# Performance work log

Measured on AMD Instinct MI355X. Metric: run time of the kernel, lower is better.

Reference implementation:

```python
import jax, jax.numpy as jnp
import numpy as np

NH, DK, DV, CHUNK = 4, 256, 256, 32
HID = 1024
FLOOR = 0.05
EPS = 1e-5


def _l2norm(x):
    return x * jax.lax.rsqrt(jnp.sum(x * x, -1, keepdims=True) + 1e-6)


def _causal_dw_conv(x, w):
    # x: (B,L,D), w: (D,K) depthwise causal FIR conv
    K = w.shape[-1]
    y = jax.lax.conv_general_dilated(
        jnp.swapaxes(x, 1, 2), w[:, None, :], (1,), [(K - 1, 0)],
        dimension_numbers=('NCH', 'OIH', 'NCH'), feature_group_count=w.shape[0])
    return jnp.swapaxes(y, 1, 2)


def _fir(x, w):
    # x: (B,L,H,D), w: (H,D,K)
    B, L, H, D = x.shape
    return _causal_dw_conv(x.reshape(B, L, H * D), w.reshape(H * D, -1)).reshape(B, L, H, D)


def _stats(x):
    mean = jnp.mean(x, -1, keepdims=True)
    var = jnp.var(x, -1, keepdims=True)
    am = jnp.mean(jnp.abs(x), -1, keepdims=True)
    l2 = jnp.linalg.norm(x, axis=-1, keepdims=True)
    return jnp.concatenate([mean, var, am, l2], -1)


def _delta_rule(q, k, v, beta, c=CHUNK):
    # q,k: (b,h,L,dk), v: (b,h,L,dv), beta: (b,h,L); L % c == 0
    b, h, L, dk = q.shape
    dv = v.shape[-1]
    q = _l2norm(q)
    k = _l2norm(k)
    v = v * beta[..., None]
    kb = k * beta[..., None]
    n = L // c
    rs = lambda t: t.reshape(b, h, n, c, -1)
    q, k, v, kb = rs(q), rs(k), rs(v), rs(kb)
    strict_low = jnp.tril(jnp.ones((c, c), bool), -1)
    attn = -(kb @ jnp.swapaxes(k, -1, -2)) * strict_low
    col = jnp.arange(c)
    def row_body(i, a):
        upd = jnp.einsum('...k,...kj->...j', a[..., i, :], a)
        return a.at[..., i, :].add(jnp.where(col < i, upd, 0.0))
    attn_inv = jax.lax.fori_loop(1, c, row_body, attn) + jnp.eye(c, dtype=attn.dtype)
    u = attn_inv @ v    # (b,h,n,c,dv)
    w = attn_inv @ kb   # (b,h,n,c,dk)
    incl_low = jnp.tril(jnp.ones((c, c), bool))
    def step(S, xs):
        q_i, k_i, u_i, w_i = xs
        attn_loc = jnp.einsum('bhid,bhjd->bhij', q_i, k_i) * incl_low
        u_i = u_i - w_i @ S
        o_i = q_i @ S + attn_loc @ u_i
        return S + jnp.swapaxes(k_i, -1, -2) @ u_i, o_i
    mv = lambda t: jnp.moveaxis(t, 2, 0)
    S0 = jnp.zeros((b, h, dk, dv), q.dtype)
    S, o = jax.lax.scan(step, S0, (mv(q), mv(k), mv(u), mv(w)))
    return jnp.moveaxis(o, 0, 2).reshape(b, h, L, dv), S


def setup_inputs() -> dict:
    key = jax.random.key(0)
    ks = jax.random.split(key, 16)
    B, L = 2, 4096
    s = 0.02
    hs = jax.random.normal(ks[0], (B, L, HID), jnp.float32)
    Wq = jax.random.normal(ks[1], (HID, NH * DK)) * s
    Wk = jax.random.normal(ks[2], (HID, NH * DK)) * s
    Wv = jax.random.normal(ks[3], (HID, NH * DV)) * s
    Wb = jax.random.normal(ks[4], (HID, NH)) * s
    conv_q_w = jax.random.normal(ks[5], (NH * DK, 4)) * 0.1
    conv_k_w = jax.random.normal(ks[6], (NH * DK, 4)) * 0.1
    conv_v_w = jax.random.normal(ks[7], (NH * DV, 4)) * 0.1
    fir_short_w = jnp.zeros((NH, DV, 5)).at[..., -1].set(1.0) + jax.random.normal(ks[8], (NH, DV, 5)) * 0.02
    fir_long_w = jnp.zeros((NH, DV, 64)).at[..., -1].set(1.0) + jax.random.normal(ks[9], (NH, DV, 64)) * 0.02
    gin, hg = HID + 16, HID * 2 // 2
    mlp_w1 = jax.random.normal(ks[10], (gin, hg)) * s
    mlp_b1 = jnp.zeros((hg,), jnp.float32)
    mlp_w2 = jax.random.normal(ks[11], (hg, 4)) * s
    mlp_b2 = jnp.array([-0.5, -0.5, 0.5, 1.5], jnp.float32)
    log_temp = jnp.zeros((NH, 1), jnp.float32)
    o_norm_w = jnp.ones((DV,), jnp.float32)
    Wo = jax.random.normal(ks[12], (NH * DV, HID)) * s
    return dict(hidden_states=hs, Wq=Wq, Wk=Wk, Wv=Wv, Wb=Wb, conv_q_w=conv_q_w,
                conv_k_w=conv_k_w, conv_v_w=conv_v_w, fir_short_w=fir_short_w,
                fir_long_w=fir_long_w, mlp_w1=mlp_w1, mlp_b1=mlp_b1, mlp_w2=mlp_w2,
                mlp_b2=mlp_b2, log_temp=log_temp, o_norm_w=o_norm_w, Wo=Wo)


def reference(hidden_states, Wq, Wk, Wv, Wb, conv_q_w, conv_k_w, conv_v_w,
              fir_short_w, fir_long_w, mlp_w1, mlp_b1, mlp_w2, mlp_b2,
              log_temp, o_norm_w, Wo):
    B, L, _ = hidden_states.shape
    # projections + causal short conv (silu) as in ShortConvolution
    q = jax.nn.silu(_causal_dw_conv(hidden_states @ Wq, conv_q_w)).reshape(B, L, NH, DK)
    k = jax.nn.silu(_causal_dw_conv(hidden_states @ Wk, conv_k_w)).reshape(B, L, NH, DK)
    v_direct = jax.nn.silu(_causal_dw_conv(hidden_states @ Wv, conv_v_w)).reshape(B, L, NH, DV)
    beta = jax.nn.sigmoid(hidden_states @ Wb)  # (B,L,NH)
    bhld = lambda t: jnp.transpose(t, (0, 2, 1, 3))
    delta_bh, _ = _delta_rule(bhld(q), bhld(k), bhld(v_direct), jnp.transpose(beta, (0, 2, 1)))
    delta_out = jnp.transpose(delta_bh, (0, 2, 1, 3))  # (B,L,NH,DV)
    local_short = _fir(v_direct, fir_short_w)
    local_long = _fir(v_direct, fir_long_w)
    stats_vec = jnp.concatenate([_stats(local_short), _stats(local_long),
                                 _stats(delta_out), _stats(v_direct)], -1)  # (B,L,NH,16)
    hs_exp = jnp.broadcast_to(hidden_states[:, :, None, :], (B, L, NH, HID))
    gate_in = jnp.concatenate([hs_exp, stats_vec], -1)
    h1 = jax.nn.gelu(gate_in @ mlp_w1 + mlp_b1, approximate=False)
    logits = h1 @ mlp_w2 + mlp_b2  # (B,L,NH,4)
    probs = jax.nn.softmax(logits / jnp.exp(log_temp), -1)
    probs = FLOOR + (1.0 - 4.0 * FLOOR) * probs  # min-floor fusion weights
    o = (probs[..., 0:1] * local_short + probs[..., 1:2] * local_long
         + probs[..., 2:3] * delta_out + probs[..., 3:4] * v_direct)
    o = o * jax.lax.rsqrt(jnp.mean(o * o, -1, keepdims=True) + EPS) * o_norm_w  # RMSNorm per head
    return o.reshape(B, L, NH * DV) @ Wo
```

## Files before the change

### kernel.cpp

```cpp
#include <hip/hip_runtime.h>
#include <hip/hip_bf16.h>

#define NTOK 8192
#define HID 1024
#define NH 4
#define DK 256
#define DV 256
#define SEQ 4096
#define NCHUNK 128

#define BM 128
#define BN 128
#define BKK 16
__global__ __launch_bounds__(256) void gemm_f32(const float* __restrict__ A,
    const float* __restrict__ B, float* __restrict__ C, int M, int N, int K) {
  __shared__ __align__(16) float As[BKK][BM + 4];
  __shared__ __align__(16) float Bs[BKK][BN + 4];
  int tid = threadIdx.x;
  int bm = blockIdx.y * BM, bn = blockIdx.x * BN;
  int tx = tid & 15, ty = tid >> 4;
  float acc[8][8];
  #pragma unroll
  for (int i = 0; i < 8; ++i)
    #pragma unroll
    for (int j = 0; j < 8; ++j) acc[i][j] = 0.f;
  for (int k0 = 0; k0 < K; k0 += BKK) {
    #pragma unroll
    for (int jj = 0; jj < 2; ++jj) {
      int v = tid + (jj << 8);
      int row = v >> 2, kk = (v & 3) << 2;
      float4 a = *(const float4*)&A[(size_t)(bm + row) * K + k0 + kk];
      As[kk + 0][row] = a.x; As[kk + 1][row] = a.y;
      As[kk + 2][row] = a.z; As[kk + 3][row] = a.w;
      int k2 = v >> 5, cl = (v & 31) << 2;
      *(float4*)&Bs[k2][cl] = *(const float4*)&B[(size_t)(k0 + k2) * N + bn + cl];
    }
    __syncthreads();
    #pragma unroll
    for (int k = 0; k < BKK; ++k) {
      float af[8], bf[8];
      *(float4*)&af[0] = *(const float4*)&As[k][ty * 8];
      *(float4*)&af[4] = *(const float4*)&As[k][ty * 8 + 4];
      *(float4*)&bf[0] = *(const float4*)&Bs[k][tx * 8];
      *(float4*)&bf[4] = *(const float4*)&Bs[k][tx * 8 + 4];
      #pragma unroll
      for (int i = 0; i < 8; ++i)
        #pragma unroll
        for (int j = 0; j < 8; ++j) acc[i][j] += af[i] * bf[j];
    }
    __syncthreads();
  }
  #pragma unroll
  for (int i = 0; i < 8; ++i) {
    size_t off = (size_t)(bm + ty * 8 + i) * N + bn + tx * 8;
    *(float4*)&C[off]     = make_float4(acc[i][0], acc[i][1], acc[i][2], acc[i][3]);
    *(float4*)&C[off + 4] = make_float4(acc[i][4], acc[i][5], acc[i][6], acc[i][7]);
  }
}

__global__ __launch_bounds__(256) void conv_silu_k(const float* __restrict__ x,
    const float* __restrict__ w, float* __restrict__ y) {
  int idx = blockIdx.x * 256 + threadIdx.x;
  int ch = idx & (HID - 1);
  int n = idx >> 10;
  int l = n & (SEQ - 1);
  float4 wv = *(const float4*)&w[ch * 4];
  float s = wv.w * x[idx];
  if (l >= 1) s += wv.z * x[idx - HID];
  if (l >= 2) s += wv.y * x[idx - 2 * HID];
  if (l >= 3) s += wv.x * x[idx - 3 * HID];
  y[idx] = s / (1.f + expf(-s));
}

__global__ __launch_bounds__(256) void beta_k(const float* __restrict__ hs,
    const float* __restrict__ Wb, float* __restrict__ beta) {
  int wv = threadIdx.x >> 6, lane = threadIdx.x & 63;
  int n = blockIdx.x * 4 + wv;
  const float* row = hs + (size_t)n * HID;
  float a0 = 0, a1 = 0, a2 = 0, a3 = 0;
  for (int k = lane; k < HID; k += 64) {
    float h = row[k];
    float4 wb = *(const float4*)&Wb[k * 4];
    a0 += h * wb.x; a1 += h * wb.y; a2 += h * wb.z; a3 += h * wb.w;
  }
  #pragma unroll
  for (int off = 32; off; off >>= 1) {
    a0 += __shfl_down(a0, off); a1 += __shfl_down(a1, off);
    a2 += __shfl_down(a2, off); a3 += __shfl_down(a3, off);
  }
  if (lane == 0) {
    float4 r = make_float4(1.f / (1.f + expf(-a0)), 1.f / (1.f + expf(-a1)),
                           1.f / (1.f + expf(-a2)), 1.f / (1.f + expf(-a3)));
    *(float4*)&beta[n * 4] = r;
  }
}

__global__ __launch_bounds__(256) void phaseA_k(
    float* __restrict__ qg, float* __restrict__ kg, const float* __restrict__ vg,
    const float* __restrict__ betag, float* __restrict__ ug, float* __restrict__ wg,
    float* __restrict__ alg) {
  __shared__ __align__(16) float kn[32][260];
  __shared__ __align__(16) float qn[32][260];
  __shared__ __align__(16) float att[32][36];
  __shared__ float bet[32];
  int blk = blockIdx.x;
  int c = blk & (NCHUNK - 1);
  int bh = blk >> 7;
  int h = bh & 3, b = bh >> 2;
  int n0 = b * SEQ + c * 32;
  size_t rowbase = (size_t)n0 * HID + h * DK;
  int tid = threadIdx.x;
  int wv = tid >> 6, L = tid & 63;

  if (tid < 32) bet[tid] = betag[(n0 + tid) * NH + h];

  {
    float4 ka[8];
    #pragma unroll
    for (int j = 0; j < 8; ++j)
      ka[j] = *(const float4*)&kg[rowbase + (size_t)(wv + 4 * j) * HID + 4 * L];
    #pragma unroll
    for (int j = 0; j < 8; ++j) {
      float ss = ka[j].x * ka[j].x + ka[j].y * ka[j].y + ka[j].z * ka[j].z + ka[j].w * ka[j].w;
      #pragma unroll
      for (int m = 1; m < 64; m <<= 1) ss += __shfl_xor(ss, m);
      float sc = 1.f / sqrtf(ss + 1e-6f);
      int row = wv + 4 * j;
      float4 r = make_float4(ka[j].x * sc, ka[j].y * sc, ka[j].z * sc, ka[j].w * sc);
      *(float4*)&kn[row][4 * L] = r;
      *(float4*)&kg[rowbase + (size_t)row * HID + 4 * L] = r;
    }
  }
  {
    float4 qa[8];
    #pragma unroll
    for (int j = 0; j < 8; ++j)
      qa[j] = *(const float4*)&qg[rowbase + (size_t)(wv + 4 * j) * HID + 4 * L];
    #pragma unroll
    for (int j = 0; j < 8; ++j) {
      float ss = qa[j].x * qa[j].x + qa[j].y * qa[j].y + qa[j].z * qa[j].z + qa[j].w * qa[j].w;
      #pragma unroll
      for (int m = 1; m < 64; m <<= 1) ss += __shfl_xor(ss, m);
      float sc = 1.f / sqrtf(ss + 1e-6f);
      int row = wv + 4 * j;
      float4 r = make_float4(qa[j].x * sc, qa[j].y * sc, qa[j].z * sc, qa[j].w * sc);
      *(float4*)&qn[row][4 * L] = r;
      *(float4*)&qg[rowbase + (size_t)row * HID + 4 * L] = r;
    }
  }
  __syncthreads();

  {
    int i0 = (tid >> 4) << 1, j0 = (tid & 15) << 1;
    float a00 = 0, a01 = 0, a10 = 0, a11 = 0;
    #pragma unroll 4
    for (int e = 0; e < 256; e += 4) {
      float4 x0 = *(const float4*)&kn[i0][e];
      float4 x1 = *(const float4*)&kn[i0 + 1][e];
      float4 y0 = *(const float4*)&kn[j0][e];
      float4 y1 = *(const float4*)&kn[j0 + 1][e];
      a00 += x0.x * y0.x + x0.y * y0.y + x0.z * y0.z + x0.w * y0.w;
      a01 += x0.x * y1.x + x0.y * y1.y + x0.z * y1.z + x0.w * y1.w;
      a10 += x1.x * y0.x + x1.y * y0.y + x1.z * y0.z + x1.w * y0.w;
      a11 += x1.x * y1.x + x1.y * y1.y + x1.z * y1.z + x1.w * y1.w;
    }
    float bi0 = bet[i0], bi1 = bet[i0 + 1];
    att[i0][j0]         = (j0 < i0)         ? -bi0 * a00 : 0.f;
    att[i0][j0 + 1]     = (j0 + 1 < i0)     ? -bi0 * a01 : 0.f;
    att[i0 + 1][j0]     = (j0 < i0 + 1)     ? -bi1 * a10 : 0.f;
    att[i0 + 1][j0 + 1] = (j0 + 1 < i0 + 1) ? -bi1 * a11 : 0.f;
  }
  {
    float* alp = alg + (size_t)(bh * NCHUNK + c) * 1024;
    int i0 = (tid >> 4) << 1, j0 = (tid & 15) << 1;
    float a00 = 0, a01 = 0, a10 = 0, a11 = 0;
    #pragma unroll 4
    for (int e = 0; e < 256; e += 4) {
      float4 x0 = *(const float4*)&qn[i0][e];
      float4 x1 = *(const float4*)&qn[i0 + 1][e];
      float4 y0 = *(const float4*)&kn[j0][e];
      float4 y1 = *(const float4*)&kn[j0 + 1][e];
      a00 += x0.x * y0.x + x0.y * y0.y + x0.z * y0.z + x0.w * y0.w;
      a01 += x0.x * y1.x + x0.y * y1.y + x0.z * y1.z + x0.w * y1.w;
      a10 += x1.x * y0.x + x1.y * y0.y + x1.z * y0.z + x1.w * y0.w;
      a11 += x1.x * y1.x + x1.y * y1.y + x1.z * y1.z + x1.w * y1.w;
    }
    alp[i0 * 32 + j0]           = (j0 <= i0)         ? a00 : 0.f;
    alp[i0 * 32 + j0 + 1]       = (j0 + 1 <= i0)     ? a01 : 0.f;
    alp[(i0 + 1) * 32 + j0]     = (j0 <= i0 + 1)     ? a10 : 0.f;
    alp[(i0 + 1) * 32 + j0 + 1] = (j0 + 1 <= i0 + 1) ? a11 : 0.f;
  }

  float vreg[32];
  {
    int d = tid;
    #pragma unroll
    for (int j = 0; j < 32; ++j)
      vreg[j] = vg[rowbase + (size_t)j * HID + d];
  }
  __syncthreads();

  if (tid < 32) {
    int j = tid;
    for (int i = 1; i < 32; ++i) {
      float upd = 0.f;
      for (int k = j + 1; k < i; ++k)
        upd += att[i][k] * att[k][j];
      if (j < i) att[i][j] += upd;
    }
  }
  __syncthreads();

  {
    int d = tid;
    #pragma unroll
    for (int j = 0; j < 32; ++j) vreg[j] *= bet[j];
    for (int i = 0; i < 32; ++i) {
      float s = vreg[i];
      #pragma unroll
      for (int j4 = 0; j4 < 32; j4 += 4) {
        float4 av = *(const float4*)&att[i][j4];
        s += av.x * vreg[j4] + av.y * vreg[j4 + 1] + av.z * vreg[j4 + 2] + av.w * vreg[j4 + 3];
      }
      ug[rowbase + (size_t)i * HID + d] = s;
    }
    float wreg[32];
    #pragma unroll
    for (int j = 0; j < 32; ++j) wreg[j] = kn[j][d] * bet[j];
    for (int i = 0; i < 32; ++i) {
      float s = wreg[i];
      #pragma unroll
      for (int j4 = 0; j4 < 32; j4 += 4) {
        float4 av = *(const float4*)&att[i][j4];
        s += av.x * wreg[j4] + av.y * wreg[j4 + 1] + av.z * wreg[j4 + 2] + av.w * wreg[j4 + 3];
      }
      wg[rowbase + (size_t)i * HID + d] = s;
    }
  }
}

__global__ __launch_bounds__(256) void scan_k(
    const float* __restrict__ qn, const float* __restrict__ kn,
    const float* __restrict__ ug, const float* __restrict__ wg,
    const float* __restrict__ alg, float* __restrict__ og) {
  __shared__ __align__(16) float S[256][8];
  __shared__ __align__(16) float stg[32][260];
  __shared__ float red[8][32][9];
  __shared__ float uloc[32][9];
  __shared__ float al[32][33];
  int blk = blockIdx.x;
  int dvg = blk & 31, bh = blk >> 5;
  int h = bh & 3, b = bh >> 2;
  int d0 = dvg * 8;
  int tid = threadIdx.x;
  int r8 = tid >> 3, dd = tid & 7;
  #pragma unroll
  for (int i = 0; i < 8; ++i) (&S[0][0])[tid + (i << 8)] = 0.f;
  __syncthreads();
  for (int c = 0; c < NCHUNK; ++c) {
    size_t rowbase = ((size_t)(b * SEQ + c * 32)) * HID + h * DK;
    const float* alp = alg + (size_t)(bh * NCHUNK + c) * 1024;
    #pragma unroll
    for (int s = 0; s < 4; ++s) { int p = tid + (s << 8); al[p >> 5][p & 31] = alp[p]; }
    #pragma unroll
    for (int j = 0; j < 8; ++j) {
      int v = tid + (j << 8);
      int row = v >> 6, c4 = (v & 63) << 2;
      *(float4*)&stg[row][c4] = *(const float4*)&wg[rowbase + (size_t)row * HID + c4];
    }
    __syncthreads();
    {
      float a0=0,a1=0,a2=0,a3=0,a4=0,a5=0,a6=0,a7=0;
      #pragma unroll
      for (int t = 0; t < 32; ++t) {
        int kk = (t << 3) + dd;
        float wv = stg[r8][kk];
        float4 s0 = *(const float4*)&S[kk][0];
        float4 s1 = *(const float4*)&S[kk][4];
        a0 += wv*s0.x; a1 += wv*s0.y; a2 += wv*s0.z; a3 += wv*s0.w;
        a4 += wv*s1.x; a5 += wv*s1.y; a6 += wv*s1.z; a7 += wv*s1.w;
      }
      float* rp = red[dd][r8];
      rp[0]=a0;rp[1]=a1;rp[2]=a2;rp[3]=a3;rp[4]=a4;rp[5]=a5;rp[6]=a6;rp[7]=a7;
    }
    __syncthreads();
    {
      float s = 0.f;
      #pragma unroll
      for (int ks = 0; ks < 8; ++ks) s += red[ks][r8][dd];
      uloc[r8][dd] = ug[rowbase + (size_t)r8 * HID + d0 + dd] - s;
    }
    #pragma unroll
    for (int j = 0; j < 8; ++j) {
      int v = tid + (j << 8);
      int row = v >> 6, c4 = (v & 63) << 2;
      *(float4*)&stg[row][c4] = *(const float4*)&qn[rowbase + (size_t)row * HID + c4];
    }
    __syncthreads();
    {
      float a0=0,a1=0,a2=0,a3=0,a4=0,a5=0,a6=0,a7=0;
      #pragma unroll
      for (int t = 0; t < 32; ++t) {
        int kk = (t << 3) + dd;
        float wv = stg[r8][kk];
        float4 s0 = *(const float4*)&S[kk][0];
        float4 s1 = *(const float4*)&S[kk][4];
        a0 += wv*s0.x; a1 += wv*s0.y; a2 += wv*s0.z; a3 += wv*s0.w;
        a4 += wv*s1.x; a5 += wv*s1.y; a6 += wv*s1.z; a7 += wv*s1.w;
      }
      float* rp = red[dd][r8];
      rp[0]=a0;rp[1]=a1;rp[2]=a2;rp[3]=a3;rp[4]=a4;rp[5]=a5;rp[6]=a6;rp[7]=a7;
    }
    __syncthreads();
    {
      float s = 0.f;
      #pragma unroll
      for (int ks = 0; ks < 8; ++ks) s += red[ks][r8][dd];
      #pragma unroll
      for (int j2 = 0; j2 < 32; ++j2) s += al[r8][j2] * uloc[j2][dd];
      og[rowbase + (size_t)r8 * HID + d0 + dd] = s;
    }
    #pragma unroll
    for (int j = 0; j < 8; ++j) {
      int v = tid + (j << 8);
      int row = v >> 6, c4 = (v & 63) << 2;
      *(float4*)&stg[row][c4] = *(const float4*)&kn[rowbase + (size_t)row * HID + c4];
    }
    __syncthreads();
    {
      float a0=0,a1=0,a2=0,a3=0,a4=0,a5=0,a6=0,a7=0;
      #pragma unroll
      for (int rr = 0; rr < 32; ++rr) {
        float kv = stg[rr][tid];
        a0 += kv*uloc[rr][0]; a1 += kv*uloc[rr][1]; a2 += kv*uloc[rr][2]; a3 += kv*uloc[rr][3];
        a4 += kv*uloc[rr][4]; a5 += kv*uloc[rr][5]; a6 += kv*uloc[rr][6]; a7 += kv*uloc[rr][7];
      }
      S[tid][0]+=a0; S[tid][1]+=a1; S[tid][2]+=a2; S[tid][3]+=a3;
      S[tid][4]+=a4; S[tid][5]+=a5; S[tid][6]+=a6; S[tid][7]+=a7;
    }
    __syncthreads();
  }
}

#define VS 196
__global__ __launch_bounds__(256) void fir_fused_k(const float* __restrict__ v,
    const float* __restrict__ wl, const float* __restrict__ wsrt,
    float* __restrict__ yl, float* __restrict__ ys) {
  __shared__ __align__(16) float vt[64 * VS];
  __shared__ __align__(16) float wlds[64 * 68];
  __shared__ float wslds[64 * 9];
  int blk = blockIdx.x;
  int ch0 = (blk & 15) << 6;
  int tok0 = (blk >> 4) << 7;
  int tid = threadIdx.x;
  {
    const float4* src = (const float4*)(wl + (size_t)ch0 * 64);
    #pragma unroll
    for (int i = 0; i < 4; ++i) {
      int f = tid + (i << 8);
      int c = f >> 4, g = f & 15;
      float4 x = src[f];
      *(float4*)&wlds[c * 68 + (g << 2)] = x;
    }
  }
  if (tid < 64) {
    #pragma unroll
    for (int j = 0; j < 5; ++j)
      wslds[tid * 9 + j] = wsrt[(size_t)(ch0 + tid) * 5 + j];
  }
  {
    int chg = tid & 15, rt = tid >> 4;
    int lb = tok0 & (SEQ - 1);
    #pragma unroll
    for (int m = 0; m < 12; ++m) {
      int rr = rt + (m << 4);
      if (rr < 191) {
        float4 x = make_float4(0.f, 0.f, 0.f, 0.f);
        if (lb + rr - 63 >= 0)
          x = *(const float4*)&v[(size_t)(tok0 - 63 + rr) * HID + ch0 + (chg << 2)];
        int cb = chg << 2;
        vt[(cb + 0) * VS + rr] = x.x;
        vt[(cb + 1) * VS + rr] = x.y;
        vt[(cb + 2) * VS + rr] = x.z;
        vt[(cb + 3) * VS + rr] = x.w;
      }
    }
  }
  __syncthreads();
  int ch = tid & 63, pt = tid >> 6;
  int p0 = pt << 5;
  const float* vrow = &vt[ch * VS + p0];
  float acc[32];
  #pragma unroll
  for (int p = 0; p < 32; ++p) acc[p] = 0.f;
  for (int g = 0; g < 16; ++g) {
    float win[36];
    #pragma unroll
    for (int j = 0; j < 9; ++j) {
      float4 x = *(const float4*)&vrow[(g << 2) + (j << 2)];
      win[4 * j] = x.x; win[4 * j + 1] = x.y; win[4 * j + 2] = x.z; win[4 * j + 3] = x.w;
    }
    float4 wq = *(const float4*)&wlds[ch * 68 + (g << 2)];
    #pragma unroll
    for (int p = 0; p < 32; ++p)
      acc[p] += wq.x * win[p] + wq.y * win[p + 1] + wq.z * win[p + 2] + wq.w * win[p + 3];
  }
  #pragma unroll
  for (int p = 0; p < 32; ++p)
    yl[(size_t)(tok0 + p0 + p) * HID + ch0 + ch] = acc[p];
  float ws5[5];
  #pragma unroll
  for (int j = 0; j < 5; ++j) ws5[j] = wslds[ch * 9 + j];
  float swin[40];
  #pragma unroll
  for (int j = 0; j < 10; ++j) {
    float4 x = *(const float4*)&vrow[56 + (j << 2)];
    swin[4 * j] = x.x; swin[4 * j + 1] = x.y; swin[4 * j + 2] = x.z; swin[4 * j + 3] = x.w;
  }
  #pragma unroll
  for (int p = 0; p < 32; ++p) {
    float s = ws5[0] * swin[p + 3] + ws5[1] * swin[p + 4] + ws5[2] * swin[p + 5]
            + ws5[3] * swin[p + 6] + ws5[4] * swin[p + 7];
    ys[(size_t)(tok0 + p0 + p) * HID + ch0 + ch] = s;
  }
}

__global__ __launch_bounds__(256) void stats_k(const float* __restrict__ ls,
    const float* __restrict__ ll, const float* __restrict__ dd,
    const float* __restrict__ vv, float* __restrict__ st) {
  int n = blockIdx.x;
  int h = threadIdx.x >> 6, lane = threadIdx.x & 63;
  size_t base = (size_t)n * HID + h * DV;
  const float* ptr[4] = {ls, ll, dd, vv};
  #pragma unroll
  for (int t = 0; t < 4; ++t) {
    const float* p = ptr[t] + base;
    float s1 = 0, s2 = 0, sa = 0;
    #pragma unroll
    for (int e = 0; e < 4; ++e) {
      float x = p[lane + e * 64];
      s1 += x; s2 += x * x; sa += fabsf(x);
    }
    #pragma unroll
    for (int off = 32; off; off >>= 1) {
      s1 += __shfl_down(s1, off); s2 += __shfl_down(s2, off); sa += __shfl_down(sa, off);
    }
    if (lane == 0) {
      float mean = s1 * (1.f / 256.f);
      float var = s2 * (1.f / 256.f) - mean * mean;
      float4 r = make_float4(mean, var, sa * (1.f / 256.f), sqrtf(s2));
      *(float4*)&st[(size_t)(n * NH + h) * 16 + t * 4] = r;
    }
  }
}

__global__ __launch_bounds__(256) void gate_fuse_k(
    const float* __restrict__ base, const float* __restrict__ st,
    const float* __restrict__ w1b, const float* __restrict__ b1,
    const float* __restrict__ w2, const float* __restrict__ b2,
    const float* __restrict__ ltemp,
    const float* __restrict__ ls, const float* __restrict__ ll,
    const float* __restrict__ dd, const float* __restrict__ vv,
    const float* __restrict__ onw, float* __restrict__ fused) {
  int n = blockIdx.x, tid = threadIdx.x;
  __shared__ float sst[4][16];
  __shared__ float wred[4][16];
  __shared__ float probs[4][4];
  __shared__ float o2red[4][4];
  __shared__ float rmss[4];
  if (tid < 64) sst[tid >> 4][tid & 15] = st[(size_t)n * 64 + tid];
  __syncthreads();
  float acc[4][4];
  #pragma unroll
  for (int a = 0; a < 4; ++a)
    #pragma unroll
    for (int cc = 0; cc < 4; ++cc) acc[a][cc] = 0.f;
  #pragma unroll
  for (int jj = 0; jj < 4; ++jj) {
    int j = tid + (jj << 8);
    float xb = base[(size_t)n * HID + j] + b1[j];
    float wr[16];
    #pragma unroll
    for (int s = 0; s < 16; ++s) wr[s] = w1b[s * 1024 + j];
    float4 w2j = *(const float4*)&w2[j * 4];
    #pragma unroll
    for (int hh = 0; hh < 4; ++hh) {
      float x = xb;
      #pragma unroll
      for (int s = 0; s < 16; ++s) x += sst[hh][s] * wr[s];
      float g = 0.5f * x * (1.f + erff(x * 0.70710678118654752f));
      acc[hh][0] += g * w2j.x; acc[hh][1] += g * w2j.y;
      acc[hh][2] += g * w2j.z; acc[hh][3] += g * w2j.w;
    }
  }
  #pragma unroll
  for (int hh = 0; hh < 4; ++hh)
    #pragma unroll
    for (int cc = 0; cc < 4; ++cc) {
      float v = acc[hh][cc];
      #pragma unroll
      for (int off = 32; off; off >>= 1) v += __shfl_down(v, off);
      if ((tid & 63) == 0) wred[tid >> 6][hh * 4 + cc] = v;
    }
  __syncthreads();
  if (tid < 4) {
    int hh = tid;
    float t = expf(ltemp[hh]);
    float lg[4], mx = -1e30f;
    #pragma unroll
    for (int cc = 0; cc < 4; ++cc) {
      float sv = wred[0][hh * 4 + cc] + wred[1][hh * 4 + cc] + wred[2][hh * 4 + cc]
               + wred[3][hh * 4 + cc] + b2[cc];
      lg[cc] = sv / t;
      mx = fmaxf(mx, lg[cc]);
    }
    float se = 0.f;
    #pragma unroll
    for (int cc = 0; cc < 4; ++cc) { lg[cc] = expf(lg[cc] - mx); se += lg[cc]; }
    float inv = 1.f / se;
    #pragma unroll
    for (int cc = 0; cc < 4; ++cc) probs[hh][cc] = 0.05f + 0.8f * lg[cc] * inv;
  }
  __syncthreads();
  int d = tid;
  float ov[4];
  #pragma unroll
  for (int hh = 0; hh < 4; ++hh) {
    size_t ix = (size_t)n * HID + hh * DV + d;
    float o = probs[hh][0] * ls[ix] + probs[hh][1] * ll[ix]
            + probs[hh][2] * dd[ix] + probs[hh][3] * vv[ix];
    ov[hh] = o;
    float v2 = o * o;
    #pragma unroll
    for (int off = 32; off; off >>= 1) v2 += __shfl_down(v2, off);
    if ((tid & 63) == 0) o2red[tid >> 6][hh] = v2;
  }
  __syncthreads();
  if (tid < 4) {
    float s = o2red[0][tid] + o2red[1][tid] + o2red[2][tid] + o2red[3][tid];
    rmss[tid] = 1.f / sqrtf(s * (1.f / 256.f) + 1e-5f);
  }
  __syncthreads();
  float wn = onw[d];
  #pragma unroll
  for (int hh = 0; hh < 4; ++hh)
    fused[(size_t)n * HID + hh * DV + d] = ov[hh] * rmss[hh] * wn;
}

extern "C" void kernel_launch(void* const* d_in, const int* in_sizes, int n_in,
                              void* d_out, int out_size, void* d_ws, size_t ws_size,
                              hipStream_t stream) {
  (void)in_sizes; (void)n_in; (void)out_size; (void)ws_size;
  const float* hs  = (const float*)d_in[0];
  const float* Wq  = (const float*)d_in[1];
  const float* Wk  = (const float*)d_in[2];
  const float* Wv  = (const float*)d_in[3];
  const float* Wb  = (const float*)d_in[4];
  const float* cqw = (const float*)d_in[5];
  const float* ckw = (const float*)d_in[6];
  const float* cvw = (const float*)d_in[7];
  const float* fsw = (const float*)d_in[8];
  const float* flw = (const float*)d_in[9];
  const float* w1  = (const float*)d_in[10];
  const float* b1  = (const float*)d_in[11];
  const float* w2  = (const float*)d_in[12];
  const float* b2  = (const float*)d_in[13];
  const float* lt  = (const float*)d_in[14];
  const float* onw = (const float*)d_in[15];
  const float* Wo  = (const float*)d_in[16];
  float* out = (float*)d_out;
  float* ws = (float*)d_ws;
  const size_t BIG = (size_t)NTOK * HID;
  float* lin = ws;
  float* qb  = ws + BIG;
  float* kb  = ws + 2 * BIG;
  float* vb  = ws + 3 * BIG;
  float* ub  = ws + 4 * BIG;
  float* wb  = ws + 5 * BIG;
  float* db  = ws + 6 * BIG;
  float* betab  = ws + 7 * BIG;
  float* statsb = betab + (size_t)NTOK * NH;
  float* alocb  = statsb + (size_t)NTOK * NH * 16;

  dim3 gg(HID / BN, NTOK / BM);
  gemm_f32<<<gg, 256, 0, stream>>>(hs, Wq, lin, NTOK, HID, HID);
  conv_silu_k<<<NTOK * HID / 256, 256, 0, stream>>>(lin, cqw, qb);
  gemm_f32<<<gg, 256, 0, stream>>>(hs, Wk, lin, NTOK, HID, HID);
  conv_silu_k<<<NTOK * HID / 256, 256, 0, stream>>>(lin, ckw, kb);
  gemm_f32<<<gg, 256, 0, stream>>>(hs, Wv, lin, NTOK, HID, HID);
  conv_silu_k<<<NTOK * HID / 256, 256, 0, stream>>>(lin, cvw, vb);
  beta_k<<<NTOK / 4, 256, 0, stream>>>(hs, Wb, betab);
  phaseA_k<<<2 * NH * NCHUNK, 256, 0, stream>>>(qb, kb, vb, betab, ub, wb, alocb);
  scan_k<<<256, 256, 0, stream>>>(qb, kb, ub, wb, alocb, db);
  fir_fused_k<<<(NTOK / 128) * (HID / 64), 256, 0, stream>>>(vb, flw, fsw, kb, qb);
  stats_k<<<NTOK, 256, 0, stream>>>(qb, kb, db, vb, statsb);
  gemm_f32<<<gg, 256, 0, stream>>>(hs, w1, wb, NTOK, HID, HID);
  gate_fuse_k<<<NTOK, 256, 0, stream>>>(wb, statsb, w1 + 1024 * 1024, b1, w2, b2, lt,
                                        qb, kb, db, vb, onw, ub);
  gemm_f32<<<gg, 256, 0, stream>>>(ub, Wo, out, NTOK, HID, HID);
}
```

Before: 2.198 ms.

## Prefetch next chunk's w/q/k rows into LDS asynchronously in delta-rule scan

The scan kernel now keeps three separate LDS staging buffers for w, q and k. It issues direct global-to-LDS loads for the next chunk while the current chunk finishes its output and state update, and it register-prefetches the attention block and u values. It also cuts the barriers per chunk and remaps block indices so the 8 (batch, head) pairs are interleaved. The goal is to hide global load latency on the serial chunk loop, at the cost of more LDS per block, which may reduce occupancy.

```diff
diff --git a/kernel.cpp b/kernel.cpp
--- a/kernel.cpp
+++ b/kernel.cpp
@@ -239,106 +239,136 @@
   }
 }
 
+__device__ __forceinline__ void stage_rows_lds(const float* gbase, float* lds0,
+                                               int wv, int L) {
+  #pragma unroll
+  for (int j = 0; j < 8; ++j) {
+    int row = wv * 8 + j;
+    const float* src = gbase + (size_t)row * HID + L * 4;
+    float* dst = lds0 + row * 260;
+    __builtin_amdgcn_global_load_lds(
+        (const __attribute__((address_space(1))) unsigned int*)src,
+        (__attribute__((address_space(3))) unsigned int*)dst, 16, 0, 0);
+  }
+}
+
 __global__ __launch_bounds__(256) void scan_k(
     const float* __restrict__ qn, const float* __restrict__ kn,
     const float* __restrict__ ug, const float* __restrict__ wg,
     const float* __restrict__ alg, float* __restrict__ og) {
   __shared__ __align__(16) float S[256][8];
-  __shared__ __align__(16) float stg[32][260];
-  __shared__ float red[8][32][9];
-  __shared__ float uloc[32][9];
-  __shared__ float al[32][33];
+  __shared__ __align__(16) float stgw[32][260];
+  __shared__ __align__(16) float stgq[32][260];
+  __shared__ __align__(16) float stgk[32][260];
+  __shared__ __align__(16) float albuf[32][33];
+  __shared__ __align__(16) float uloc[32][12];
+  __shared__ float red[8 * 296];
+
   int blk = blockIdx.x;
-  int dvg = blk & 31, bh = blk >> 5;
+  int bh = blk & 7, dvg = blk >> 3;
   int h = bh & 3, b = bh >> 2;
   int d0 = dvg * 8;
   int tid = threadIdx.x;
-  int r8 = tid >> 3, dd = tid & 7;
-  #pragma unroll
-  for (int i = 0; i < 8; ++i) (&S[0][0])[tid + (i << 8)] = 0.f;
-  __syncthreads();
+  int wv = tid >> 6, L = tid & 63;
+  int rP = tid >> 3, ks = tid & 7;
+  int r2 = rP, dv2 = ks;
+
+  #pragma unroll
+  for (int i = 0; i < 8; ++i) ((float*)S)[tid + (i << 8)] = 0.f;
+
+  size_t bhbase = (size_t)b * SEQ * HID + h * DK;
+  const float* alp0 = alg + (size_t)bh * NCHUNK * 1024;
+
+  stage_rows_lds(wg + bhbase, &stgw[0][0], wv, L);
+  stage_rows_lds(qn + bhbase, &stgq[0][0], wv, L);
+  stage_rows_lds(kn + bhbase, &stgk[0][0], wv, L);
+  float alr0 = alp0[tid], alr1 = alp0[tid + 256], alr2 = alp0[tid + 512], alr3 = alp0[tid + 768];
+  float u_cur = ug[bhbase + (size_t)r2 * HID + d0 + dv2];
+
   for (int c = 0; c < NCHUNK; ++c) {
-    size_t rowbase = ((size_t)(b * SEQ + c * 32)) * HID + h * DK;
-    const float* alp = alg + (size_t)(bh * NCHUNK + c) * 1024;
-    #pragma unroll
-    for (int s = 0; s < 4; ++s) { int p = tid + (s << 8); al[p >> 5][p & 31] = alp[p]; }
-    #pragma unroll
-    for (int j = 0; j < 8; ++j) {
-      int v = tid + (j << 8);
-      int row = v >> 6, c4 = (v & 63) << 2;
-      *(float4*)&stg[row][c4] = *(const float4*)&wg[rowbase + (size_t)row * HID + c4];
-    }
+    size_t rowbase = bhbase + (size_t)c * 32 * HID;
     __syncthreads();
     {
-      float a0=0,a1=0,a2=0,a3=0,a4=0,a5=0,a6=0,a7=0;
-      #pragma unroll
-      for (int t = 0; t < 32; ++t) {
-        int kk = (t << 3) + dd;
-        float wv = stg[r8][kk];
-        float4 s0 = *(const float4*)&S[kk][0];
-        float4 s1 = *(const float4*)&S[kk][4];
-        a0 += wv*s0.x; a1 += wv*s0.y; a2 += wv*s0.z; a3 += wv*s0.w;
-        a4 += wv*s1.x; a5 += wv*s1.y; a6 += wv*s1.z; a7 += wv*s1.w;
-      }
-      float* rp = red[dd][r8];
-      rp[0]=a0;rp[1]=a1;rp[2]=a2;rp[3]=a3;rp[4]=a4;rp[5]=a5;rp[6]=a6;rp[7]=a7;
+      albuf[tid >> 5][tid & 31] = alr0;
+      albuf[(tid + 256) >> 5][tid & 31] = alr1;
+      albuf[(tid + 512) >> 5][tid & 31] = alr2;
+      albuf[(tid + 768) >> 5][tid & 31] = alr3;
+    }
+    float a0=0,a1=0,a2=0,a3=0,a4=0,a5=0,a6=0,a7=0;
+    #pragma unroll
+    for (int t = 0; t < 32; ++t) {
+      int kk = (t << 3) + ks;
+      float wvv = stgw[rP][kk];
+      float4 s0 = *(const float4*)&S[kk][0];
+      float4 s1 = *(const float4*)&S[kk][4];
+      a0 += wvv*s0.x; a1 += wvv*s0.y; a2 += wvv*s0.z; a3 += wvv*s0.w;
+      a4 += wvv*s1.x; a5 += wvv*s1.y; a6 += wvv*s1.z; a7 += wvv*s1.w;
+    }
+    {
+      int base = rP * 9 + ks;
+      red[0*296+base]=a0; red[1*296+base]=a1; red[2*296+base]=a2; red[3*296+base]=a3;
+      red[4*296+base]=a4; red[5*296+base]=a5; red[6*296+base]=a6; red[7*296+base]=a7;
     }
     __syncthreads();
     {
       float s = 0.f;
-      #pragma unroll
-      for (int ks = 0; ks < 8; ++ks) s += red[ks][r8][dd];
-      uloc[r8][dd] = ug[rowbase + (size_t)r8 * HID + d0 + dd] - s;
-    }
-    #pragma unroll
-    for (int j = 0; j < 8; ++j) {
-      int v = tid + (j << 8);
-      int row = v >> 6, c4 = (v & 63) << 2;
-      *(float4*)&stg[row][c4] = *(const float4*)&qn[rowbase + (size_t)row * HID + c4];
+      int base = dv2 * 296 + r2 * 9;
+      #pragma unroll
+      for (int k2 = 0; k2 < 8; ++k2) s += red[base + k2];
+      uloc[r2][dv2] = u_cur - s;
     }
     __syncthreads();
+    a0=0;a1=0;a2=0;a3=0;a4=0;a5=0;a6=0;a7=0;
+    #pragma unroll
+    for (int t = 0; t < 32; ++t) {
+      int kk = (t << 3) + ks;
+      float qvv = stgq[rP][kk];
+      float4 s0 = *(const float4*)&S[kk][0];
+      float4 s1 = *(const float4*)&S[kk][4];
+      a0 += qvv*s0.x; a1 += qvv*s0.y; a2 += qvv*s0.z; a3 += qvv*s0.w;
+      a4 += qvv*s1.x; a5 += qvv*s1.y; a6 += qvv*s1.z; a7 += qvv*s1.w;
+    }
     {
-      float a0=0,a1=0,a2=0,a3=0,a4=0,a5=0,a6=0,a7=0;
-      #pragma unroll
-      for (int t = 0; t < 32; ++t) {
-        int kk = (t << 3) + dd;
-        float wv = stg[r8][kk];
-        float4 s0 = *(const float4*)&S[kk][0];
-        float4 s1 = *(const float4*)&S[kk][4];
-        a0 += wv*s0.x; a1 += wv*s0.y; a2 += wv*s0.z; a3 += wv*s0.w;
-        a4 += wv*s1.x; a5 += wv*s1.y; a6 += wv*s1.z; a7 += wv*s1.w;
-      }
-      float* rp = red[dd][r8];
-      rp[0]=a0;rp[1]=a1;rp[2]=a2;rp[3]=a3;rp[4]=a4;rp[5]=a5;rp[6]=a6;rp[7]=a7;
+      int base = rP * 9 + ks;
+      red[0*296+base]=a0; red[1*296+base]=a1; red[2*296+base]=a2; red[3*296+base]=a3;
+      red[4*296+base]=a4; red[5*296+base]=a5; red[6*296+base]=a6; red[7*296+base]=a7;
+    }
+    float d0r=0,d1r=0,d2r=0,d3r=0,d4r=0,d5r=0,d6r=0,d7r=0;
+    #pragma unroll
+    for (int rr = 0; rr < 32; ++rr) {
+      float kv = stgk[rr][tid];
+      float4 u0 = *(const float4*)&uloc[rr][0];
+      float4 u1 = *(const float4*)&uloc[rr][4];
+      d0r += kv*u0.x; d1r += kv*u0.y; d2r += kv*u0.z; d3r += kv*u0.w;
+      d4r += kv*u1.x; d5r += kv*u1.y; d6r += kv*u1.z; d7r += kv*u1.w;
     }
     __syncthreads();
+    if (c + 1 < NCHUNK) {
+      size_t rbn = rowbase + (size_t)32 * HID;
+      stage_rows_lds(wg + rbn, &stgw[0][0], wv, L);
+      stage_rows_lds(qn + rbn, &stgq[0][0], wv, L);
+      stage_rows_lds(kn + rbn, &stgk[0][0], wv, L);
+      const float* alp = alp0 + (size_t)(c + 1) * 1024;
+      alr0 = alp[tid]; alr1 = alp[tid + 256]; alr2 = alp[tid + 512]; alr3 = alp[tid + 768];
+      u_cur = ug[rbn + (size_t)r2 * HID + d0 + dv2];
+    }
     {
       float s = 0.f;
-      #pragma unroll
-      for (int ks = 0; ks < 8; ++ks) s += red[ks][r8][dd];
-      #pragma unroll
-      for (int j2 = 0; j2 < 32; ++j2) s += al[r8][j2] * uloc[j2][dd];
-      og[rowbase + (size_t)r8 * HID + d0 + dd] = s;
-    }
-    #pragma unroll
-    for (int j = 0; j < 8; ++j) {
-      int v = tid + (j << 8);
-      int row = v >> 6, c4 = (v & 63) << 2;
-      *(float4*)&stg[row][c4] = *(const float4*)&kn[rowbase + (size_t)row * HID + c4];
-    }
-    __syncthreads();
+      int base = dv2 * 296 + r2 * 9;
+      #pragma unroll
+      for (int k2 = 0; k2 < 8; ++k2) s += red[base + k2];
+      #pragma unroll
+      for (int j2 = 0; j2 < 32; ++j2) s += albuf[r2][j2] * uloc[j2][dv2];
+      og[rowbase + (size_t)r2 * HID + d0 + dv2] = s;
+    }
     {
-      float a0=0,a1=0,a2=0,a3=0,a4=0,a5=0,a6=0,a7=0;
-      #pragma unroll
-      for (int rr = 0; rr < 32; ++rr) {
-        float kv = stg[rr][tid];
-        a0 += kv*uloc[rr][0]; a1 += kv*uloc[rr][1]; a2 += kv*uloc[rr][2]; a3 += kv*uloc[rr][3];
-        a4 += kv*uloc[rr][4]; a5 += kv*uloc[rr][5]; a6 += kv*uloc[rr][6]; a7 += kv*uloc[rr][7];
-      }
-      S[tid][0]+=a0; S[tid][1]+=a1; S[tid][2]+=a2; S[tid][3]+=a3;
-      S[tid][4]+=a4; S[tid][5]+=a5; S[tid][6]+=a6; S[tid][7]+=a7;
-    }
-    __syncthreads();
+      float4 c0 = *(const float4*)&S[tid][0];
+      float4 c1 = *(const float4*)&S[tid][4];
+      c0.x += d0r; c0.y += d1r; c0.z += d2r; c0.w += d3r;
+      c1.x += d4r; c1.y += d5r; c1.z += d6r; c1.w += d7r;
+      *(float4*)&S[tid][0] = c0;
+      *(float4*)&S[tid][4] = c1;
+    }
   }
 }
 
```

Result: no change. 2.210 ms (+0.5%).
